# Performance work log

Hardware: AMD Instinct MI355X
Metric: run time of the kernel (lower is better)

The kernel has to match this reference:

```python
import jax, jax.numpy as jnp
import numpy as np

B, T, F, U = 64, 512, 32, 64
EPS = 1e-3  # keras LayerNormalization default epsilon


def _ln(x, g, b):
    m = jnp.mean(x, axis=-1, keepdims=True)
    v = jnp.var(x, axis=-1, keepdims=True)
    return (x - m) / jnp.sqrt(v + EPS) * g + b


def setup_inputs() -> dict:
    key = jax.random.key(0)
    ks = jax.random.split(key, 24)
    s = 0.05
    inp = {
        "x": jax.random.normal(ks[0], (B, T, F), dtype=jnp.float32),
        # per-feature GRNs, stacked over F (each sub-net has independent params)
        "W1": jax.random.normal(ks[1], (F, U), jnp.float32) * s,   # dense_1 (1->U)
        "b1": jnp.zeros((F, U), jnp.float32),
        "W2": jax.random.normal(ks[2], (F, U, U), jnp.float32) * s,  # dense_2 (U->U)
        "b2": jnp.zeros((F, U), jnp.float32),
        "Wg1": jax.random.normal(ks[3], (F, U, U), jnp.float32) * s,  # GLU linear
        "bg1": jnp.zeros((F, U), jnp.float32),
        "Wg2": jax.random.normal(ks[4], (F, U, U), jnp.float32) * s,  # GLU gate
        "bg2": jnp.zeros((F, U), jnp.float32),
        "Wp": jax.random.normal(ks[5], (F, U), jnp.float32) * s,   # project (1->U)
        "bp": jnp.zeros((F, U), jnp.float32),
        "gamma": jnp.ones((F, U), jnp.float32),
        "beta": jnp.zeros((F, U), jnp.float32),
        # weights GRN (F -> F, no projection since in_dim == units == F)
        "w1w": jax.random.normal(ks[6], (F, F), jnp.float32) * s,
        "b1w": jnp.zeros((F,), jnp.float32),
        "w2w": jax.random.normal(ks[7], (F, F), jnp.float32) * s,
        "b2w": jnp.zeros((F,), jnp.float32),
        "wg1w": jax.random.normal(ks[8], (F, F), jnp.float32) * s,
        "bg1w": jnp.zeros((F,), jnp.float32),
        "wg2w": jax.random.normal(ks[9], (F, F), jnp.float32) * s,
        "bg2w": jnp.zeros((F,), jnp.float32),
        "gammaw": jnp.ones((F,), jnp.float32),
        "betaw": jnp.zeros((F,), jnp.float32),
    }
    return inp


def reference(x, W1, b1, W2, b2, Wg1, bg1, Wg2, bg2, Wp, bp, gamma, beta,
              w1w, b1w, w2w, b2w, wg1w, bg1w, wg2w, bg2w, gammaw, betaw):
    # ---- variable weights GRN on flattened features (input dim F == units F, no projection) ----
    h = jax.nn.elu(jnp.einsum('btf,fg->btg', x, w1w) + b1w)
    h = jnp.einsum('btf,fg->btg', h, w2w) + b2w
    g = (jnp.einsum('btf,fg->btg', h, wg1w) + bg1w) * jax.nn.sigmoid(
        jnp.einsum('btf,fg->btg', h, wg2w) + bg2w)
    w = _ln(g + x, gammaw, betaw)
    w = jax.nn.softmax(w, axis=-1)  # [B,T,F]

    # ---- per-feature GRNs, batched over F (scalar input per feature) ----
    xe = x[..., None]                                   # [B,T,F,1]
    res = xe * Wp + bp                                  # project residual [B,T,F,U]
    h = jax.nn.elu(xe * W1 + b1)                        # dense_1 [B,T,F,U]
    h = jnp.einsum('btfu,fuv->btfv', h, W2) + b2        # dense_2
    g = (jnp.einsum('btfu,fuv->btfv', h, Wg1) + bg1) * jax.nn.sigmoid(
        jnp.einsum('btfu,fuv->btfv', h, Wg2) + bg2)     # GLU
    y = _ln(g + res, gamma, beta)                       # [B,T,F,U]

    out = jnp.einsum('btfu,btf->btu', y, w)             # softmax-weighted sum over features
    return out, w
```

## Files before the change

### kernel.cpp

```cpp
#include <hip/hip_runtime.h>
#include <hip/hip_bf16.h>


typedef float f4      __attribute__((ext_vector_type(4)));
typedef float f2      __attribute__((ext_vector_type(2)));
typedef float f32x4   __attribute__((ext_vector_type(4)));
typedef short bf16x8  __attribute__((ext_vector_type(8)));
typedef unsigned short u16x8 __attribute__((ext_vector_type(8)));

#define N_ROWS 32768
#define F_DIM  32
#define U_DIM  64
#define RPB    16
#define NTHR   256
#define NBLK   (N_ROWS / RPB)

#define X_OFF   0
#define WT_OFF  2304
#define PW_OFF  3584
#define VA_OFF  11776
#define HX_OFF  12544
#define SMEM_BYTES 19968

__device__ __forceinline__ unsigned short bfu(float x) {
  union { __hip_bfloat16 h; unsigned short u; } c;
  c.h = __float2bfloat16(x);
  return c.u;
}
__device__ __forceinline__ float bf2f(unsigned short u) {
  union { float f; unsigned v; } c; c.v = ((unsigned)u) << 16; return c.f;
}

__global__ __launch_bounds__(256) void vsn_prep(
    const float* __restrict__ W2,  const float* __restrict__ Wg1, const float* __restrict__ Wg2,
    const float* __restrict__ W1,  const float* __restrict__ b1,  const float* __restrict__ b2,
    const float* __restrict__ bg1, const float* __restrict__ bg2,
    const float* __restrict__ Wp,  const float* __restrict__ bp,
    const float* __restrict__ gamma_, const float* __restrict__ beta_,
    unsigned short* __restrict__ wtg, float* __restrict__ vect)
{
  const int t = threadIdx.x, blk = blockIdx.x;
  if (blk < 192) {
    const int m = blk >> 6;
    const int f = (blk >> 1) & 31;
    const int half = blk & 1;
    const float* src = (m == 0) ? W2 : (m == 1) ? Wg1 : Wg2;
    src += f * 4096;
    const int c  = half * 256 + t;
    const int nt = c >> 7;
    const int rr = c & 127;
    const int kt = rr >> 6;
    const int ln = rr & 63;
    const int g  = ln >> 4, lrr = ln & 15;
    const int uo = lrr + 16 * nt;
    u16x8 tmp;
    if (m == 0) {
      #pragma unroll
      for (int j = 0; j < 8; ++j)
        tmp[j] = bfu(src[(8 * g + 32 * kt + j) * 64 + uo]);
    } else {
      #pragma unroll
      for (int j = 0; j < 8; ++j)
        tmp[j] = bfu(src[(4 * g + (j & 3) + 16 * (j >> 2) + 32 * kt) * 64 + uo]);
    }
    *(u16x8*)(wtg + ((size_t)(m * 32 + f) * 512 + c) * 8) = tmp;
  } else {
    const int h = blk - 192;
    for (int i = h * 1024 + t; i < (h + 1) * 1024; i += 256) {
      const int f = i >> 6, u = i & 63;
      float* vf = vect + f * 576;
      vf[u]              = W1[i];
      vf[64 + u]         = b1[i];
      vf[128 + u]        = b2[i];
      vf[192 + u * 4 + 0] = bg1[i];
      vf[192 + u * 4 + 1] = bg2[i];
      vf[192 + u * 4 + 2] = Wp[i];
      vf[192 + u * 4 + 3] = bp[i];
      vf[448 + u * 2 + 0] = gamma_[i];
      vf[448 + u * 2 + 1] = beta_[i];
    }
  }
}

__global__ __launch_bounds__(NTHR, 4) void vsn_main(
    const float* __restrict__ x,
    const unsigned short* __restrict__ wtg,
    const float* __restrict__ vect,
    const float* __restrict__ w1w, const float* __restrict__ w2w,
    const float* __restrict__ wg1w, const float* __restrict__ wg2w,
    const float* __restrict__ b1w, const float* __restrict__ b2w,
    const float* __restrict__ bg1w, const float* __restrict__ bg2w,
    const float* __restrict__ gammaw, const float* __restrict__ betaw,
    float* __restrict__ out, float* __restrict__ wout)
{
  __shared__ __align__(16) char smem[SMEM_BYTES];
  const int t  = threadIdx.x;
  const int r0 = blockIdx.x * RPB;

  float* xt  = (float*)(smem + X_OFF);
  unsigned short* wtlb = (unsigned short*)(smem + WT_OFF);
  float* wA  = (float*)(smem + PW_OFF);
  float* vAl = (float*)(smem + VA_OFF);
  float* hex = (float*)(smem + HX_OFF);

  const int wid  = t >> 6;
  const int lane = t & 63;
  const int lr   = lane & 15;
  const int lg   = lane >> 4;
  const int fbase = wid * 8;

  if (t < 128) {
    f4 v = ((const f4*)(x + (size_t)r0 * F_DIM))[t];
    *((f4*)(xt + (t >> 3) * 36 + ((t & 7) << 2))) = v;
  }

  const f4* vect4 = (const f4*)vect;
  f4 rv0 = vect4[fbase * 144 + lane];
  f4 rv1 = vect4[fbase * 144 + 64 + lane];
  f4 rv2 = {};
  if (lane < 16) rv2 = vect4[fbase * 144 + 128 + lane];

  #pragma unroll
  for (int i = 0; i < 2; ++i) {
    int i4 = t + i * NTHR;
    int m = i4 >> 8, off = (i4 & 255) << 2;
    const float* src = m ? w2w : w1w;
    *(f4*)(wA + m * 1024 + off) = *((const f4*)(src + off));
  }
  if (t < 48) {
    int m = t >> 3, off = (t & 7) << 2;
    const float* src = (m==0)?b1w:(m==1)?b2w:(m==2)?bg1w:(m==3)?bg2w:(m==4)?gammaw:betaw;
    *(f4*)(vAl + m * 32 + off) = *((const f4*)(src + off));
  }
  __syncthreads();

  {
    const int ar = t >> 4;
    const int g0 = (t & 15) << 1;

    f2 hacc = { vAl[g0], vAl[g0 + 1] };
    #pragma unroll
    for (int ff = 0; ff < 32; ++ff) {
      float xv = xt[ar * 36 + ff];
      f2 w0 = *(const f2*)(wA + ff * 32 + g0);
      hacc.x += xv * w0.x; hacc.y += xv * w0.y;
    }
    hacc.x = hacc.x > 0.f ? hacc.x : (__expf(hacc.x) - 1.f);
    hacc.y = hacc.y > 0.f ? hacc.y : (__expf(hacc.y) - 1.f);
    *(f2*)(hex + ar * 36 + g0) = hacc;
    __syncthreads();

    f2 h2acc = { vAl[32 + g0], vAl[32 + g0 + 1] };
    #pragma unroll
    for (int ff = 0; ff < 32; ++ff) {
      float hv = hex[ar * 36 + ff];
      f2 w0 = *(const f2*)(wA + 1024 + ff * 32 + g0);
      h2acc.x += hv * w0.x; h2acc.y += hv * w0.y;
    }
    __syncthreads();
    *(f2*)(hex + ar * 36 + g0) = h2acc;
    #pragma unroll
    for (int i = 0; i < 2; ++i) {
      int i4 = t + i * NTHR;
      int m = i4 >> 8, off = (i4 & 255) << 2;
      const float* src = m ? wg2w : wg1w;
      *(f4*)(wA + m * 1024 + off) = *((const f4*)(src + off));
    }
    __syncthreads();

    f2 aacc = { vAl[64 + g0], vAl[64 + g0 + 1] };
    f2 bacc = { vAl[96 + g0], vAl[96 + g0 + 1] };
    #pragma unroll
    for (int ff = 0; ff < 32; ++ff) {
      float hv = hex[ar * 36 + ff];
      f2 wa0 = *(const f2*)(wA + ff * 32 + g0);
      f2 wb0 = *(const f2*)(wA + 1024 + ff * 32 + g0);
      aacc.x += hv * wa0.x; aacc.y += hv * wa0.y;
      bacc.x += hv * wb0.x; bacc.y += hv * wb0.y;
    }
    f2 zz;
    {
      float sgx = __builtin_amdgcn_rcpf(1.f + __expf(-bacc.x));
      float sgy = __builtin_amdgcn_rcpf(1.f + __expf(-bacc.y));
      zz.x = aacc.x * sgx + xt[ar * 36 + g0];
      zz.y = aacc.y * sgy + xt[ar * 36 + g0 + 1];
    }
    __syncthreads();
    *(f2*)(hex + ar * 36 + g0) = zz;
    __syncthreads();

    float s1 = 0.f, s2 = 0.f;
    #pragma unroll
    for (int ff = 0; ff < 32; ++ff) { float z = hex[ar * 36 + ff]; s1 += z; s2 += z * z; }
    float mA = s1 * 0.03125f;
    float vA = s2 * 0.03125f - mA * mA;
    float rsA = __builtin_amdgcn_rsqf(vA + 1e-3f);
    float mx = -1e30f;
    #pragma unroll
    for (int ff = 0; ff < 32; ++ff) {
      float y = (hex[ar * 36 + ff] - mA) * rsA * vAl[128 + ff] + vAl[160 + ff];
      mx = fmaxf(mx, y);
    }
    float es = 0.f;
    #pragma unroll
    for (int ff = 0; ff < 32; ++ff) {
      float y = (hex[ar * 36 + ff] - mA) * rsA * vAl[128 + ff] + vAl[160 + ff];
      es += __expf(y - mx);
    }
    float inv = __builtin_amdgcn_rcpf(es);
    float w0 = __expf((hex[ar * 36 + g0] - mA) * rsA * vAl[128 + g0] + vAl[160 + g0] - mx) * inv;
    float w1_ = __expf((hex[ar * 36 + g0 + 1] - mA) * rsA * vAl[128 + g0 + 1] + vAl[160 + g0 + 1] - mx) * inv;
    unsigned wu = (unsigned)bfu(w0) | ((unsigned)bfu(w1_) << 16);
    *(unsigned*)(wtlb + ar * 40 + g0) = wu;
    *(f2*)(wout + (size_t)(r0 + ar) * 32 + g0) = (f2){w0, w1_};
    __syncthreads();
  }

  f4* vst4 = ((f4*)(smem + PW_OFF)) + wid * 144;
  float* vsc = (float*)(smem + PW_OFF) + wid * 576;

  vst4[lane] = rv0; vst4[64 + lane] = rv1;
  if (lane < 16) vst4[128 + lane] = rv2;

  const bf16x8* wf = (const bf16x8*)wtg;

  f32x4 acc[4];
  #pragma unroll
  for (int nt = 0; nt < 4; ++nt) acc[nt] = (f32x4){0.f, 0.f, 0.f, 0.f};

  for (int i = 0; i < 8; ++i) {
    const int f = fbase + i;

    const int base0 = (0 * 32 + f) * 512 + lane;
    bf16x8 w2f[8];
    #pragma unroll
    for (int nt = 0; nt < 4; ++nt)
      #pragma unroll
      for (int kt = 0; kt < 2; ++kt)
        w2f[nt * 2 + kt] = wf[base0 + nt * 128 + kt * 64];

    const float s_ = xt[lr * 36 + f];
    bf16x8 afr[2];
    #pragma unroll
    for (int kt = 0; kt < 2; ++kt) {
      const int u0 = 8 * lg + 32 * kt;
      f4 wa  = *(const f4*)(vsc + u0);
      f4 wb_ = *(const f4*)(vsc + u0 + 4);
      f4 ba  = *(const f4*)(vsc + 64 + u0);
      f4 bb_ = *(const f4*)(vsc + 64 + u0 + 4);
      bf16x8 af;
      #pragma unroll
      for (int j = 0; j < 4; ++j) {
        float h = s_ * wa[j] + ba[j];
        h = h > 0.f ? h : (__expf(h) - 1.f);
        af[j] = (short)bfu(h);
      }
      #pragma unroll
      for (int j = 0; j < 4; ++j) {
        float h = s_ * wb_[j] + bb_[j];
        h = h > 0.f ? h : (__expf(h) - 1.f);
        af[4 + j] = (short)bfu(h);
      }
      afr[kt] = af;
    }

    f32x4 c1[4];
    #pragma unroll
    for (int nt = 0; nt < 4; ++nt) {
      c1[nt] = (f32x4){0.f, 0.f, 0.f, 0.f};
      #pragma unroll
      for (int kt = 0; kt < 2; ++kt)
        c1[nt] = __builtin_amdgcn_mfma_f32_16x16x32_bf16(w2f[nt * 2 + kt], afr[kt], c1[nt], 0, 0, 0);
    }

    f4 b2q[4];
    #pragma unroll
    for (int kt = 0; kt < 2; ++kt)
      #pragma unroll
      for (int n2 = 0; n2 < 2; ++n2)
        b2q[n2 + 2 * kt] = *(const f4*)(vsc + 128 + 4 * lg + 16 * n2 + 32 * kt);
    bf16x8 a2[2];
    #pragma unroll
    for (int kt = 0; kt < 2; ++kt) {
      bf16x8 af;
      #pragma unroll
      for (int j = 0; j < 8; ++j) {
        const int q = (j >> 2) + 2 * kt;
        af[j] = (short)bfu(c1[q][j & 3] + b2q[q][j & 3]);
      }
      a2[kt] = af;
    }

    const int base1 = (1 * 32 + f) * 512 + lane;
    bf16x8 bfa[8];
    #pragma unroll
    for (int nt = 0; nt < 4; ++nt)
      #pragma unroll
      for (int kt = 0; kt < 2; ++kt)
        bfa[nt * 2 + kt] = wf[base1 + nt * 128 + kt * 64];
    f32x4 ca[4], cb[4];
    #pragma unroll
    for (int nt = 0; nt < 4; ++nt) {
      ca[nt] = (f32x4){0.f,0.f,0.f,0.f};
      #pragma unroll
      for (int kt = 0; kt < 2; ++kt)
        ca[nt] = __builtin_amdgcn_mfma_f32_16x16x32_bf16(a2[kt], bfa[nt * 2 + kt], ca[nt], 0, 0, 0);
    }

    const int base2 = (2 * 32 + f) * 512 + lane;
    bf16x8 bfb[8];
    #pragma unroll
    for (int nt = 0; nt < 4; ++nt)
      #pragma unroll
      for (int kt = 0; kt < 2; ++kt)
        bfb[nt * 2 + kt] = wf[base2 + nt * 128 + kt * 64];
    #pragma unroll
    for (int nt = 0; nt < 4; ++nt) {
      cb[nt] = (f32x4){0.f,0.f,0.f,0.f};
      #pragma unroll
      for (int kt = 0; kt < 2; ++kt)
        cb[nt] = __builtin_amdgcn_mfma_f32_16x16x32_bf16(a2[kt], bfb[nt * 2 + kt], cb[nt], 0, 0, 0);
    }

    if (i < 7) {
      rv0 = vect4[(f + 1) * 144 + lane];
      rv1 = vect4[(f + 1) * 144 + 64 + lane];
      if (lane < 16) rv2 = vect4[(f + 1) * 144 + 128 + lane];
    }

    float xr[4], wr[4];
    #pragma unroll
    for (int rg = 0; rg < 4; ++rg) {
      const int rl = 4 * lg + rg;
      xr[rg] = xt[rl * 36 + f];
      wr[rg] = bf2f(wtlb[rl * 40 + f]);
    }
    float zf[4][4];
    float s1[4] = {0.f,0.f,0.f,0.f}, s2[4] = {0.f,0.f,0.f,0.f};
    #pragma unroll
    for (int nt = 0; nt < 4; ++nt) {
      const int u = lr + 16 * nt;
      f4 Q = *(const f4*)(vsc + 192 + u * 4);
      #pragma unroll
      for (int rg = 0; rg < 4; ++rg) {
        float a = ca[nt][rg] + Q[0];
        float b = cb[nt][rg] + Q[1];
        float sg = __builtin_amdgcn_rcpf(1.f + __expf(-b));
        float z = a * sg + (xr[rg] * Q[2] + Q[3]);
        zf[nt][rg] = z;
        s1[rg] += z;
        s2[rg] += z * z;
      }
    }
    #pragma unroll
    for (int rg = 0; rg < 4; ++rg) {
      #pragma unroll
      for (int m = 1; m < 16; m <<= 1) {
        s1[rg] += __shfl_xor(s1[rg], m, 64);
        s2[rg] += __shfl_xor(s2[rg], m, 64);
      }
    }
    float rswr[4], nc2[4];
    #pragma unroll
    for (int rg = 0; rg < 4; ++rg) {
      float mn = s1[rg] * 0.015625f;
      float var = s2[rg] * 0.015625f - mn * mn;
      float rs = __builtin_amdgcn_rsqf(var + 1e-3f);
      rswr[rg] = rs * wr[rg];
      nc2[rg]  = -mn * rswr[rg];
    }
    #pragma unroll
    for (int nt = 0; nt < 4; ++nt) {
      const int u = lr + 16 * nt;
      f2 G = *(const f2*)(vsc + 448 + u * 2);
      #pragma unroll
      for (int rg = 0; rg < 4; ++rg) {
        float tm = rswr[rg] * zf[nt][rg] + nc2[rg];
        acc[nt][rg] += G.x * tm + G.y * wr[rg];
      }
    }

    if (i < 7) {
      vst4[lane] = rv0; vst4[64 + lane] = rv1;
      if (lane < 16) vst4[128 + lane] = rv2;
    }
  }

  __syncthreads();
  float* cmb = (float*)(smem + PW_OFF);
  #pragma unroll
  for (int nt = 0; nt < 4; ++nt)
    #pragma unroll
    for (int rg = 0; rg < 4; ++rg)
      cmb[wid * 1024 + (4 * lg + rg) * 64 + lr + 16 * nt] = acc[nt][rg];
  __syncthreads();
  {
    const f4* cmb4 = (const f4*)cmb;
    f4 o = cmb4[t] + cmb4[256 + t] + cmb4[512 + t] + cmb4[768 + t];
    ((f4*)(out + (size_t)r0 * U_DIM))[t] = o;
  }
}

extern "C" void kernel_launch(void* const* d_in, const int* in_sizes, int n_in,
                              void* d_out, int out_size, void* d_ws, size_t ws_size,
                              hipStream_t stream)
{
  (void)in_sizes; (void)n_in; (void)out_size; (void)ws_size;
  const float* x    = (const float*)d_in[0];
  const float* W1   = (const float*)d_in[1];
  const float* b1   = (const float*)d_in[2];
  const float* W2   = (const float*)d_in[3];
  const float* b2   = (const float*)d_in[4];
  const float* Wg1  = (const float*)d_in[5];
  const float* bg1  = (const float*)d_in[6];
  const float* Wg2  = (const float*)d_in[7];
  const float* bg2  = (const float*)d_in[8];
  const float* Wp   = (const float*)d_in[9];
  const float* bp   = (const float*)d_in[10];
  const float* gm   = (const float*)d_in[11];
  const float* bt   = (const float*)d_in[12];
  const float* w1w  = (const float*)d_in[13];
  const float* b1w  = (const float*)d_in[14];
  const float* w2w  = (const float*)d_in[15];
  const float* b2w  = (const float*)d_in[16];
  const float* wg1w = (const float*)d_in[17];
  const float* bg1w = (const float*)d_in[18];
  const float* wg2w = (const float*)d_in[19];
  const float* bg2w = (const float*)d_in[20];
  const float* gmw  = (const float*)d_in[21];
  const float* btw  = (const float*)d_in[22];

  unsigned short* wtg = (unsigned short*)d_ws;
  float* vect = (float*)((char*)d_ws + 786432);

  float* out  = (float*)d_out;
  float* wout = out + (size_t)N_ROWS * U_DIM;

  vsn_prep<<<194, 256, 0, stream>>>(W2, Wg1, Wg2, W1, b1, b2, bg1, bg2, Wp, bp, gm, bt, wtg, vect);
  vsn_main<<<NBLK, NTHR, 0, stream>>>(x, wtg, vect, w1w, w2w, wg1w, wg2w,
                                      b1w, b2w, bg1w, bg2w, gmw, btw, out, wout);
}
```

Measured before the change: 197.5 us.

## Compute weights GRN with bf16 MFMA and read per-feature vectors from global

The feature-weight GRN (four 32x32 matmuls, LayerNorm and softmax) used to run as scalar FP32 FMAs over shared memory with several block barriers. It now runs on bf16 MFMA fragments that the prep kernel builds in advance, with LN and softmax reductions done through lane shuffles. The per-feature vector staging in LDS is also removed; the main loop reads those values straight from global memory, which shrinks shared memory and drops barriers. In exchange the weights path loses precision to bf16, and the output weights are now rounded through bf16 before being written.

```diff
diff --git a/kernel.cpp b/kernel.cpp
--- a/kernel.cpp
+++ b/kernel.cpp
@@ -6,6 +6,7 @@
 typedef float f2      __attribute__((ext_vector_type(2)));
 typedef float f32x4   __attribute__((ext_vector_type(4)));
 typedef short bf16x8  __attribute__((ext_vector_type(8)));
+typedef unsigned short u16x4 __attribute__((ext_vector_type(4)));
 typedef unsigned short u16x8 __attribute__((ext_vector_type(8)));
 
 #define N_ROWS 32768
@@ -15,12 +16,13 @@
 #define NTHR   256
 #define NBLK   (N_ROWS / RPB)
 
+#define PHA_FRAG 49152
+#define VECT_BYTE_OFF 794624
+
 #define X_OFF   0
 #define WT_OFF  2304
-#define PW_OFF  3584
-#define VA_OFF  11776
-#define HX_OFF  12544
-#define SMEM_BYTES 19968
+#define VA_OFF  3584
+#define SMEM_BYTES 16384
 
 __device__ __forceinline__ unsigned short bfu(float x) {
   union { __hip_bfloat16 h; unsigned short u; } c;
@@ -37,6 +39,8 @@
     const float* __restrict__ bg1, const float* __restrict__ bg2,
     const float* __restrict__ Wp,  const float* __restrict__ bp,
     const float* __restrict__ gamma_, const float* __restrict__ beta_,
+    const float* __restrict__ w1w, const float* __restrict__ w2w,
+    const float* __restrict__ wg1w, const float* __restrict__ wg2w,
     unsigned short* __restrict__ wtg, float* __restrict__ vect)
 {
   const int t = threadIdx.x, blk = blockIdx.x;
@@ -64,7 +68,7 @@
         tmp[j] = bfu(src[(4 * g + (j & 3) + 16 * (j >> 2) + 32 * kt) * 64 + uo]);
     }
     *(u16x8*)(wtg + ((size_t)(m * 32 + f) * 512 + c) * 8) = tmp;
-  } else {
+  } else if (blk < 194) {
     const int h = blk - 192;
     for (int i = h * 1024 + t; i < (h + 1) * 1024; i += 256) {
       const int f = i >> 6, u = i & 63;
@@ -79,6 +83,27 @@
       vf[448 + u * 2 + 0] = gamma_[i];
       vf[448 + u * 2 + 1] = beta_[i];
     }
+  } else {
+    #pragma unroll
+    for (int cc = 0; cc < 2; ++cc) {
+      const int q = t + cc * 256;
+      const int mat = q >> 7;
+      const int nt  = (q >> 6) & 1;
+      const int ln  = q & 63;
+      const int lr  = ln & 15, lg = ln >> 4;
+      const float* src = (mat == 0) ? w1w : (mat == 1) ? w2w : (mat == 2) ? wg1w : wg2w;
+      u16x8 tmp;
+      if (mat == 0) {
+        #pragma unroll
+        for (int j = 0; j < 8; ++j)
+          tmp[j] = bfu(src[(8 * lg + j) * 32 + lr + 16 * nt]);
+      } else {
+        #pragma unroll
+        for (int j = 0; j < 8; ++j)
+          tmp[j] = bfu(src[(4 * lg + (j & 3) + 16 * (j >> 2)) * 32 + lr + 16 * nt]);
+      }
+      *(u16x8*)(wtg + ((size_t)PHA_FRAG + q) * 8) = tmp;
+    }
   }
 }
 
@@ -86,8 +111,6 @@
     const float* __restrict__ x,
     const unsigned short* __restrict__ wtg,
     const float* __restrict__ vect,
-    const float* __restrict__ w1w, const float* __restrict__ w2w,
-    const float* __restrict__ wg1w, const float* __restrict__ wg2w,
     const float* __restrict__ b1w, const float* __restrict__ b2w,
     const float* __restrict__ bg1w, const float* __restrict__ bg2w,
     const float* __restrict__ gammaw, const float* __restrict__ betaw,
@@ -99,9 +122,7 @@
 
   float* xt  = (float*)(smem + X_OFF);
   unsigned short* wtlb = (unsigned short*)(smem + WT_OFF);
-  float* wA  = (float*)(smem + PW_OFF);
   float* vAl = (float*)(smem + VA_OFF);
-  float* hex = (float*)(smem + HX_OFF);
 
   const int wid  = t >> 6;
   const int lane = t & 63;
@@ -113,20 +134,6 @@
     f4 v = ((const f4*)(x + (size_t)r0 * F_DIM))[t];
     *((f4*)(xt + (t >> 3) * 36 + ((t & 7) << 2))) = v;
   }
-
-  const f4* vect4 = (const f4*)vect;
-  f4 rv0 = vect4[fbase * 144 + lane];
-  f4 rv1 = vect4[fbase * 144 + 64 + lane];
-  f4 rv2 = {};
-  if (lane < 16) rv2 = vect4[fbase * 144 + 128 + lane];
-
-  #pragma unroll
-  for (int i = 0; i < 2; ++i) {
-    int i4 = t + i * NTHR;
-    int m = i4 >> 8, off = (i4 & 255) << 2;
-    const float* src = m ? w2w : w1w;
-    *(f4*)(wA + m * 1024 + off) = *((const f4*)(src + off));
-  }
   if (t < 48) {
     int m = t >> 3, off = (t & 7) << 2;
     const float* src = (m==0)?b1w:(m==1)?b2w:(m==2)?bg1w:(m==3)?bg2w:(m==4)?gammaw:betaw;
@@ -135,92 +142,104 @@
   __syncthreads();
 
   {
-    const int ar = t >> 4;
-    const int g0 = (t & 15) << 1;
-
-    f2 hacc = { vAl[g0], vAl[g0 + 1] };
-    #pragma unroll
-    for (int ff = 0; ff < 32; ++ff) {
-      float xv = xt[ar * 36 + ff];
-      f2 w0 = *(const f2*)(wA + ff * 32 + g0);
-      hacc.x += xv * w0.x; hacc.y += xv * w0.y;
-    }
-    hacc.x = hacc.x > 0.f ? hacc.x : (__expf(hacc.x) - 1.f);
-    hacc.y = hacc.y > 0.f ? hacc.y : (__expf(hacc.y) - 1.f);
-    *(f2*)(hex + ar * 36 + g0) = hacc;
-    __syncthreads();
-
-    f2 h2acc = { vAl[32 + g0], vAl[32 + g0 + 1] };
-    #pragma unroll
-    for (int ff = 0; ff < 32; ++ff) {
-      float hv = hex[ar * 36 + ff];
-      f2 w0 = *(const f2*)(wA + 1024 + ff * 32 + g0);
-      h2acc.x += hv * w0.x; h2acc.y += hv * w0.y;
-    }
-    __syncthreads();
-    *(f2*)(hex + ar * 36 + g0) = h2acc;
-    #pragma unroll
-    for (int i = 0; i < 2; ++i) {
-      int i4 = t + i * NTHR;
-      int m = i4 >> 8, off = (i4 & 255) << 2;
-      const float* src = m ? wg2w : wg1w;
-      *(f4*)(wA + m * 1024 + off) = *((const f4*)(src + off));
-    }
-    __syncthreads();
-
-    f2 aacc = { vAl[64 + g0], vAl[64 + g0 + 1] };
-    f2 bacc = { vAl[96 + g0], vAl[96 + g0 + 1] };
-    #pragma unroll
-    for (int ff = 0; ff < 32; ++ff) {
-      float hv = hex[ar * 36 + ff];
-      f2 wa0 = *(const f2*)(wA + ff * 32 + g0);
-      f2 wb0 = *(const f2*)(wA + 1024 + ff * 32 + g0);
-      aacc.x += hv * wa0.x; aacc.y += hv * wa0.y;
-      bacc.x += hv * wb0.x; bacc.y += hv * wb0.y;
-    }
-    f2 zz;
-    {
-      float sgx = __builtin_amdgcn_rcpf(1.f + __expf(-bacc.x));
-      float sgy = __builtin_amdgcn_rcpf(1.f + __expf(-bacc.y));
-      zz.x = aacc.x * sgx + xt[ar * 36 + g0];
-      zz.y = aacc.y * sgy + xt[ar * 36 + g0 + 1];
-    }
-    __syncthreads();
-    *(f2*)(hex + ar * 36 + g0) = zz;
-    __syncthreads();
-
+    const bf16x8* pf = ((const bf16x8*)wtg) + PHA_FRAG;
+
+    f4 xa0 = *(const f4*)(xt + lr * 36 + 8 * lg);
+    f4 xa1 = *(const f4*)(xt + lr * 36 + 8 * lg + 4);
+    bf16x8 xb;
+    #pragma unroll
+    for (int j = 0; j < 4; ++j) { xb[j] = (short)bfu(xa0[j]); xb[4 + j] = (short)bfu(xa1[j]); }
+
+    f32x4 c1a[2];
+    #pragma unroll
+    for (int nt = 0; nt < 2; ++nt)
+      c1a[nt] = __builtin_amdgcn_mfma_f32_16x16x32_bf16(
+          pf[(0 * 2 + nt) * 64 + lane], xb, (f32x4){0.f,0.f,0.f,0.f}, 0, 0, 0);
+    float hv[8];
+    #pragma unroll
+    for (int nt = 0; nt < 2; ++nt)
+      #pragma unroll
+      for (int rg = 0; rg < 4; ++rg) {
+        const int g = 4 * lg + rg + 16 * nt;
+        float h = c1a[nt][rg] + vAl[g];
+        hv[nt * 4 + rg] = h > 0.f ? h : (__expf(h) - 1.f);
+      }
+    bf16x8 hf;
+    #pragma unroll
+    for (int j = 0; j < 8; ++j) hf[j] = (short)bfu(hv[j]);
+
+    f32x4 c2a[2];
+    #pragma unroll
+    for (int nt = 0; nt < 2; ++nt)
+      c2a[nt] = __builtin_amdgcn_mfma_f32_16x16x32_bf16(
+          pf[(1 * 2 + nt) * 64 + lane], hf, (f32x4){0.f,0.f,0.f,0.f}, 0, 0, 0);
+    bf16x8 h2f;
+    #pragma unroll
+    for (int nt = 0; nt < 2; ++nt)
+      #pragma unroll
+      for (int rg = 0; rg < 4; ++rg) {
+        const int g = 4 * lg + rg + 16 * nt;
+        h2f[nt * 4 + rg] = (short)bfu(c2a[nt][rg] + vAl[32 + g]);
+      }
+
+    f32x4 cga[2], cgb[2];
+    #pragma unroll
+    for (int nt = 0; nt < 2; ++nt) {
+      cga[nt] = __builtin_amdgcn_mfma_f32_16x16x32_bf16(
+          pf[(2 * 2 + nt) * 64 + lane], h2f, (f32x4){0.f,0.f,0.f,0.f}, 0, 0, 0);
+      cgb[nt] = __builtin_amdgcn_mfma_f32_16x16x32_bf16(
+          pf[(3 * 2 + nt) * 64 + lane], h2f, (f32x4){0.f,0.f,0.f,0.f}, 0, 0, 0);
+    }
+    float zv[8];
     float s1 = 0.f, s2 = 0.f;
     #pragma unroll
-    for (int ff = 0; ff < 32; ++ff) { float z = hex[ar * 36 + ff]; s1 += z; s2 += z * z; }
-    float mA = s1 * 0.03125f;
-    float vA = s2 * 0.03125f - mA * mA;
-    float rsA = __builtin_amdgcn_rsqf(vA + 1e-3f);
-    float mx = -1e30f;
-    #pragma unroll
-    for (int ff = 0; ff < 32; ++ff) {
-      float y = (hex[ar * 36 + ff] - mA) * rsA * vAl[128 + ff] + vAl[160 + ff];
-      mx = fmaxf(mx, y);
-    }
-    float es = 0.f;
-    #pragma unroll
-    for (int ff = 0; ff < 32; ++ff) {
-      float y = (hex[ar * 36 + ff] - mA) * rsA * vAl[128 + ff] + vAl[160 + ff];
-      es += __expf(y - mx);
-    }
-    float inv = __builtin_amdgcn_rcpf(es);
-    float w0 = __expf((hex[ar * 36 + g0] - mA) * rsA * vAl[128 + g0] + vAl[160 + g0] - mx) * inv;
-    float w1_ = __expf((hex[ar * 36 + g0 + 1] - mA) * rsA * vAl[128 + g0 + 1] + vAl[160 + g0 + 1] - mx) * inv;
-    unsigned wu = (unsigned)bfu(w0) | ((unsigned)bfu(w1_) << 16);
-    *(unsigned*)(wtlb + ar * 40 + g0) = wu;
-    *(f2*)(wout + (size_t)(r0 + ar) * 32 + g0) = (f2){w0, w1_};
-    __syncthreads();
-  }
-
-  f4* vst4 = ((f4*)(smem + PW_OFF)) + wid * 144;
-  float* vsc = (float*)(smem + PW_OFF) + wid * 576;
-
-  vst4[lane] = rv0; vst4[64 + lane] = rv1;
-  if (lane < 16) vst4[128 + lane] = rv2;
+    for (int nt = 0; nt < 2; ++nt)
+      #pragma unroll
+      for (int rg = 0; rg < 4; ++rg) {
+        const int g = 4 * lg + rg + 16 * nt;
+        float a = cga[nt][rg] + vAl[64 + g];
+        float b = cgb[nt][rg] + vAl[96 + g];
+        float sg = __builtin_amdgcn_rcpf(1.f + __expf(-b));
+        float z = a * sg + xt[lr * 36 + g];
+        zv[nt * 4 + rg] = z;
+        s1 += z; s2 += z * z;
+      }
+    s1 += __shfl_xor(s1, 16, 64); s1 += __shfl_xor(s1, 32, 64);
+    s2 += __shfl_xor(s2, 16, 64); s2 += __shfl_xor(s2, 32, 64);
+    const float mA = s1 * 0.03125f;
+    const float vA = s2 * 0.03125f - mA * mA;
+    const float rsA = __builtin_amdgcn_rsqf(vA + 1e-3f);
+    float yv[8], mx = -1e30f;
+    #pragma unroll
+    for (int nt = 0; nt < 2; ++nt)
+      #pragma unroll
+      for (int rg = 0; rg < 4; ++rg) {
+        const int g = 4 * lg + rg + 16 * nt;
+        float y = (zv[nt * 4 + rg] - mA) * rsA * vAl[128 + g] + vAl[160 + g];
+        yv[nt * 4 + rg] = y;
+        mx = fmaxf(mx, y);
+      }
+    mx = fmaxf(mx, __shfl_xor(mx, 16, 64));
+    mx = fmaxf(mx, __shfl_xor(mx, 32, 64));
+    float ev[8], es = 0.f;
+    #pragma unroll
+    for (int j = 0; j < 8; ++j) { ev[j] = __expf(yv[j] - mx); es += ev[j]; }
+    es += __shfl_xor(es, 16, 64); es += __shfl_xor(es, 32, 64);
+    const float inv = __builtin_amdgcn_rcpf(es);
+    #pragma unroll
+    for (int nt = 0; nt < 2; ++nt)
+      #pragma unroll
+      for (int rg = 0; rg < 4; ++rg) {
+        const int g = 4 * lg + rg + 16 * nt;
+        wtlb[lr * 40 + g] = bfu(ev[nt * 4 + rg] * inv);
+      }
+    if (t < 128) {
+      const int row = t >> 3, c4 = (t & 7) << 2;
+      u16x4 wq = *(const u16x4*)(wtlb + row * 40 + c4);
+      f4 wo = { bf2f(wq[0]), bf2f(wq[1]), bf2f(wq[2]), bf2f(wq[3]) };
+      *(f4*)(wout + (size_t)(r0 + row) * 32 + c4) = wo;
+    }
+  }
 
   const bf16x8* wf = (const bf16x8*)wtg;
 
@@ -230,6 +249,7 @@
 
   for (int i = 0; i < 8; ++i) {
     const int f = fbase + i;
+    const float* vb = vect + f * 576;
 
     const int base0 = (0 * 32 + f) * 512 + lane;
     bf16x8 w2f[8];
@@ -244,10 +264,10 @@
     #pragma unroll
     for (int kt = 0; kt < 2; ++kt) {
       const int u0 = 8 * lg + 32 * kt;
-      f4 wa  = *(const f4*)(vsc + u0);
-      f4 wb_ = *(const f4*)(vsc + u0 + 4);
-      f4 ba  = *(const f4*)(vsc + 64 + u0);
-      f4 bb_ = *(const f4*)(vsc + 64 + u0 + 4);
+      f4 wa  = *(const f4*)(vb + u0);
+      f4 wb_ = *(const f4*)(vb + u0 + 4);
+      f4 ba  = *(const f4*)(vb + 64 + u0);
+      f4 bb_ = *(const f4*)(vb + 64 + u0 + 4);
       bf16x8 af;
       #pragma unroll
       for (int j = 0; j < 4; ++j) {
@@ -278,7 +298,7 @@
     for (int kt = 0; kt < 2; ++kt)
       #pragma unroll
       for (int n2 = 0; n2 < 2; ++n2)
-        b2q[n2 + 2 * kt] = *(const f4*)(vsc + 128 + 4 * lg + 16 * n2 + 32 * kt);
+        b2q[n2 + 2 * kt] = *(const f4*)(vb + 128 + 4 * lg + 16 * n2 + 32 * kt);
     bf16x8 a2[2];
     #pragma unroll
     for (int kt = 0; kt < 2; ++kt) {
@@ -320,12 +340,6 @@
       #pragma unroll
       for (int kt = 0; kt < 2; ++kt)
         cb[nt] = __builtin_amdgcn_mfma_f32_16x16x32_bf16(a2[kt], bfb[nt * 2 + kt], cb[nt], 0, 0, 0);
-    }
-
-    if (i < 7) {
-      rv0 = vect4[(f + 1) * 144 + lane];
-      rv1 = vect4[(f + 1) * 144 + 64 + lane];
-      if (lane < 16) rv2 = vect4[(f + 1) * 144 + 128 + lane];
     }
 
     float xr[4], wr[4];
@@ -340,7 +354,7 @@
     #pragma unroll
     for (int nt = 0; nt < 4; ++nt) {
       const int u = lr + 16 * nt;
-      f4 Q = *(const f4*)(vsc + 192 + u * 4);
+      f4 Q = *(const f4*)(vb + 192 + u * 4);
       #pragma unroll
       for (int rg = 0; rg < 4; ++rg) {
         float a = ca[nt][rg] + Q[0];
@@ -372,22 +386,17 @@
     #pragma unroll
     for (int nt = 0; nt < 4; ++nt) {
       const int u = lr + 16 * nt;
-      f2 G = *(const f2*)(vsc + 448 + u * 2);
+      f2 G = *(const f2*)(vb + 448 + u * 2);
       #pragma unroll
       for (int rg = 0; rg < 4; ++rg) {
         float tm = rswr[rg] * zf[nt][rg] + nc2[rg];
         acc[nt][rg] += G.x * tm + G.y * wr[rg];
       }
     }
-
-    if (i < 7) {
-      vst4[lane] = rv0; vst4[64 + lane] = rv1;
-      if (lane < 16) vst4[128 + lane] = rv2;
-    }
   }
 
   __syncthreads();
-  float* cmb = (float*)(smem + PW_OFF);
+  float* cmb = (float*)smem;
   #pragma unroll
   for (int nt = 0; nt < 4; ++nt)
     #pragma unroll
@@ -431,12 +440,13 @@
   const float* btw  = (const float*)d_in[22];
 
   unsigned short* wtg = (unsigned short*)d_ws;
-  float* vect = (float*)((char*)d_ws + 786432);
+  float* vect = (float*)((char*)d_ws + VECT_BYTE_OFF);
 
   float* out  = (float*)d_out;
   float* wout = out + (size_t)N_ROWS * U_DIM;
 
-  vsn_prep<<<194, 256, 0, stream>>>(W2, Wg1, Wg2, W1, b1, b2, bg1, bg2, Wp, bp, gm, bt, wtg, vect);
-  vsn_main<<<NBLK, NTHR, 0, stream>>>(x, wtg, vect, w1w, w2w, wg1w, wg2w,
+  vsn_prep<<<195, 256, 0, stream>>>(W2, Wg1, Wg2, W1, b1, b2, bg1, bg2, Wp, bp, gm, bt,
+                                    w1w, w2w, wg1w, wg2w, wtg, vect);
+  vsn_main<<<NBLK, NTHR, 0, stream>>>(x, wtg, vect,
                                       b1w, b2w, bg1w, bg2w, gmw, btw, out, wout);
 }
```

Result: slower. 214.7 us (+8.7%).
